# Kernel tuning notes

Measured on AMD Instinct MI355X. Metric: run time of the kernel, lower is better.

## Reference

```python
import jax, jax.numpy as jnp
import numpy as np

HIDDEN = 2048
N_HEADS = 16
N_KV = 2
HEAD_DIM = HIDDEN // N_HEADS  # 128


def setup_inputs() -> dict:
    key = jax.random.key(0)
    ks = jax.random.split(key, 9)
    s = 0.02
    kv_dim = N_KV * HEAD_DIM
    return {
        "hidden_states": jax.random.normal(ks[0], (2, 2048, HIDDEN), jnp.float32),
        "Wq": jax.random.normal(ks[1], (HIDDEN, HIDDEN), jnp.float32) * s,
        "bq": jnp.zeros((HIDDEN,), jnp.float32),
        "Wk": jax.random.normal(ks[2], (HIDDEN, kv_dim), jnp.float32) * s,
        "bk": jnp.zeros((kv_dim,), jnp.float32),
        "Wv": jax.random.normal(ks[3], (HIDDEN, kv_dim), jnp.float32) * s,
        "bv": jnp.zeros((kv_dim,), jnp.float32),
        "Wo": jax.random.normal(ks[4], (HIDDEN, HIDDEN), jnp.float32) * s,
        "bo": jnp.zeros((HIDDEN,), jnp.float32),
    }


def reference(hidden_states, Wq, bq, Wk, bk, Wv, bv, Wo, bo):
    B, S, _ = hidden_states.shape
    scaling = HEAD_DIM ** (-0.5)
    rep = N_HEADS // N_KV

    q = hidden_states @ Wq + bq                      # [B,S,H*D]
    k = hidden_states @ Wk + bk                      # [B,S,KV*D]
    v = hidden_states @ Wv + bv

    q = q.reshape(B, S, N_HEADS, HEAD_DIM) * scaling
    k = k.reshape(B, S, N_KV, HEAD_DIM)
    v = v.reshape(B, S, N_KV, HEAD_DIM)
    # repeat_interleave KV heads to match query heads (faithful to source)
    k = jnp.repeat(k, rep, axis=2)                   # [B,S,H,D]
    v = jnp.repeat(v, rep, axis=2)

    attn = jnp.einsum('bqhd,bkhd->bhqk', q, k)       # [B,H,S,S] score matrix
    attn = jax.nn.softmax(attn, axis=-1)
    out = jnp.einsum('bhqk,bkhd->bqhd', attn, v)     # [B,S,H,D]
    out = out.reshape(B, S, N_HEADS * HEAD_DIM)
    return out @ Wo + bo
```

## Files before the change

### kernel.cpp

```cpp
#include <hip/hip_runtime.h>

typedef __bf16 bf16;
typedef __bf16 bf16x4 __attribute__((ext_vector_type(4)));
typedef __bf16 bf16x8 __attribute__((ext_vector_type(8)));
typedef float  f32x4  __attribute__((ext_vector_type(4)));

#define AS1 __attribute__((address_space(1)))
#define AS3 __attribute__((address_space(3)))

__device__ __forceinline__ void gload_lds16(const void* g, void* l) {
    __builtin_amdgcn_global_load_lds((const AS1 void*)g, (AS3 void*)l, 16, 0, 0);
}

__global__ __launch_bounds__(256) void prep(
    const float* __restrict__ X,  const float* __restrict__ Wq,
    const float* __restrict__ Wk, const float* __restrict__ Wv,
    const float* __restrict__ Wo, const float* __restrict__ bq,
    const float* __restrict__ bk, const float* __restrict__ bv,
    bf16* __restrict__ Xb, bf16* __restrict__ Wqkvt,
    bf16* __restrict__ Wot, float* __restrict__ bqkv)
{
    __shared__ float tile[32][33];
    int bid = blockIdx.x;
    if (bid < 8192) {
        int i = bid * 256 + threadIdx.x;
        float4 v = ((const float4*)X)[i];
        bf16x4 o = { (bf16)v.x, (bf16)v.y, (bf16)v.z, (bf16)v.w };
        ((bf16x4*)Xb)[i] = o;
        return;
    }
    bid -= 8192;
    const float* src; bf16* dst; int R, C, bx, by;
    if (bid < 4096)      { src = Wq; dst = Wqkvt;                      R = 2048; C = 2048; bx = bid & 63; by = bid >> 6; }
    else if (bid < 4608) { int t = bid - 4096; src = Wk; dst = Wqkvt + (size_t)2048 * 2048; R = 2048; C = 256; bx = t & 7; by = t >> 3; }
    else if (bid < 5120) { int t = bid - 4608; src = Wv; dst = Wqkvt + (size_t)2304 * 2048; R = 2048; C = 256; bx = t & 7; by = t >> 3; }
    else if (bid < 9216) { int t = bid - 5120; src = Wo; dst = Wot;    R = 2048; C = 2048; bx = t & 63; by = t >> 6; }
    else {
        int i = (bid - 9216) * 256 + threadIdx.x;
        if (i < 2048) bqkv[i] = bq[i];
        else if (i < 2304) bqkv[i] = bk[i - 2048];
        else if (i < 2560) bqkv[i] = bv[i - 2304];
        return;
    }
    int tx = threadIdx.x & 31, tg = threadIdx.x >> 5;
    int c0 = bx * 32, r0 = by * 32;
    #pragma unroll
    for (int j = tg; j < 32; j += 8)
        tile[j][tx] = src[(size_t)(r0 + j) * C + c0 + tx];
    __syncthreads();
    #pragma unroll
    for (int j = tg; j < 32; j += 8)
        dst[(size_t)(c0 + j) * R + r0 + tx] = (bf16)tile[tx][j];
}

template<int OUTBF>
__global__ __launch_bounds__(256) void gemm_bt(
    const bf16* __restrict__ A, const bf16* __restrict__ Bt,
    const float* __restrict__ bias, void* __restrict__ Cv,
    int M, int N, int K, float scale)
{
    __shared__ bf16 As[128 * 32];
    __shared__ bf16 Bs[128 * 32];
    const int tid = threadIdx.x;
    const int l = tid & 63, w = tid >> 6;
    const int wm = w >> 1, wn = w & 1;
    const size_t rowBase = (size_t)blockIdx.y * 128;
    const size_t colBase = (size_t)blockIdx.x * 128;

    f32x4 acc[4][4] = {};

    const int srow = l >> 2;
    const int schunk = (l & 3) ^ ((l >> 3) & 3);
    const int frow = l & 15;
    const int fswz = (frow >> 1) & 3;
    const int g = l >> 4;

    const bf16* Ag = A  + (rowBase + w * 32 + srow) * (size_t)K + schunk * 8;
    const bf16* Bg = Bt + (colBase + w * 32 + srow) * (size_t)K + schunk * 8;

    for (int k0 = 0; k0 < K; k0 += 32) {
        gload_lds16(Ag + k0,                  As + (w * 32) * 32);
        gload_lds16(Ag + 16 * (size_t)K + k0, As + (w * 32 + 16) * 32);
        gload_lds16(Bg + k0,                  Bs + (w * 32) * 32);
        gload_lds16(Bg + 16 * (size_t)K + k0, Bs + (w * 32 + 16) * 32);
        __syncthreads();

        bf16x8 af[4], bfr[4];
        #pragma unroll
        for (int mi = 0; mi < 4; ++mi)
            af[mi] = *(const bf16x8*)(As + (wm * 64 + mi * 16 + frow) * 32 + ((g ^ fswz) << 3));
        #pragma unroll
        for (int ni = 0; ni < 4; ++ni)
            bfr[ni] = *(const bf16x8*)(Bs + (wn * 64 + ni * 16 + frow) * 32 + ((g ^ fswz) << 3));
        #pragma unroll
        for (int mi = 0; mi < 4; ++mi)
            #pragma unroll
            for (int ni = 0; ni < 4; ++ni)
                acc[mi][ni] = __builtin_amdgcn_mfma_f32_16x16x32_bf16(af[mi], bfr[ni], acc[mi][ni], 0, 0, 0);
        __syncthreads();
    }

    const int cr = (l >> 4) * 4;
    const int cc = l & 15;
    #pragma unroll
    for (int ni = 0; ni < 4; ++ni) {
        const int col = (int)colBase + wn * 64 + ni * 16 + cc;
        const float bv = bias[col];
        #pragma unroll
        for (int mi = 0; mi < 4; ++mi) {
            #pragma unroll
            for (int r = 0; r < 4; ++r) {
                const size_t row = rowBase + wm * 64 + mi * 16 + cr + r;
                float v = (acc[mi][ni][r] + bv) * scale;
                if (OUTBF) ((bf16*)Cv)[row * N + col] = (bf16)v;
                else       ((float*)Cv)[row * N + col] = v;
            }
        }
    }
}

__global__ __launch_bounds__(256) void gemm_qkv(
    const bf16* __restrict__ A, const bf16* __restrict__ Bt,
    const float* __restrict__ bias, bf16* __restrict__ Qb, bf16* __restrict__ Kb,
    bf16* __restrict__ VT, float qscale)
{
    constexpr int K = 2048;
    __shared__ bf16 As[128 * 32];
    __shared__ bf16 Bs[128 * 32];
    const int tid = threadIdx.x;
    const int l = tid & 63, w = tid >> 6;
    const int wm = w >> 1, wn = w & 1;
    const size_t rowBase = (size_t)blockIdx.y * 128;
    const size_t colBase = (size_t)blockIdx.x * 128;

    f32x4 acc[4][4] = {};

    const int srow = l >> 2;
    const int schunk = (l & 3) ^ ((l >> 3) & 3);
    const int frow = l & 15;
    const int fswz = (frow >> 1) & 3;
    const int g = l >> 4;

    const bf16* Ag = A  + (rowBase + w * 32 + srow) * (size_t)K + schunk * 8;
    const bf16* Bg = Bt + (colBase + w * 32 + srow) * (size_t)K + schunk * 8;

    for (int k0 = 0; k0 < K; k0 += 32) {
        gload_lds16(Ag + k0,                  As + (w * 32) * 32);
        gload_lds16(Ag + 16 * (size_t)K + k0, As + (w * 32 + 16) * 32);
        gload_lds16(Bg + k0,                  Bs + (w * 32) * 32);
        gload_lds16(Bg + 16 * (size_t)K + k0, Bs + (w * 32 + 16) * 32);
        __syncthreads();

        bf16x8 af[4], bfr[4];
        #pragma unroll
        for (int mi = 0; mi < 4; ++mi)
            af[mi] = *(const bf16x8*)(As + (wm * 64 + mi * 16 + frow) * 32 + ((g ^ fswz) << 3));
        #pragma unroll
        for (int ni = 0; ni < 4; ++ni)
            bfr[ni] = *(const bf16x8*)(Bs + (wn * 64 + ni * 16 + frow) * 32 + ((g ^ fswz) << 3));
        #pragma unroll
        for (int mi = 0; mi < 4; ++mi)
            #pragma unroll
            for (int ni = 0; ni < 4; ++ni)
                acc[mi][ni] = __builtin_amdgcn_mfma_f32_16x16x32_bf16(af[mi], bfr[ni], acc[mi][ni], 0, 0, 0);
        __syncthreads();
    }

    const int cr = (l >> 4) * 4;
    const int cc = l & 15;
    const int cb = (int)colBase;
    #pragma unroll
    for (int ni = 0; ni < 4; ++ni) {
        const int col = cb + wn * 64 + ni * 16 + cc;
        const float bv = bias[col];
        if (cb < 2048) {
            #pragma unroll
            for (int mi = 0; mi < 4; ++mi)
                #pragma unroll
                for (int r = 0; r < 4; ++r) {
                    const size_t row = rowBase + wm * 64 + mi * 16 + cr + r;
                    Qb[row * 2048 + col] = (bf16)((acc[mi][ni][r] + bv) * qscale);
                }
        } else if (cb < 2304) {
            #pragma unroll
            for (int mi = 0; mi < 4; ++mi)
                #pragma unroll
                for (int r = 0; r < 4; ++r) {
                    const size_t row = rowBase + wm * 64 + mi * 16 + cr + r;
                    Kb[row * 256 + (col - 2048)] = (bf16)(acc[mi][ni][r] + bv);
                }
        } else {
            const int vcol = col - 2304;
            const int kvh = vcol >> 7, d = vcol & 127;
            #pragma unroll
            for (int mi = 0; mi < 4; ++mi) {
                const size_t row0 = rowBase + wm * 64 + mi * 16 + cr;
                const int bb = (int)(row0 >> 11);
                const int s  = (int)(row0 & 2047);
                const int tile = s >> 6, sp = s & 63;
                const int slot = (sp & 35) | ((sp & 8) << 1) | ((sp & 4) << 1) | ((sp & 16) >> 2);
                bf16x4 v4 = { (bf16)(acc[mi][ni][0] + bv), (bf16)(acc[mi][ni][1] + bv),
                              (bf16)(acc[mi][ni][2] + bv), (bf16)(acc[mi][ni][3] + bv) };
                *(bf16x4*)(VT + ((size_t)((bb * 2 + kvh) * 128 + d)) * 2048 + tile * 64 + slot) = v4;
            }
        }
    }
}

__global__ __launch_bounds__(512, 4) void attn_fwd(
    const bf16* __restrict__ Q, const bf16* __restrict__ Kb,
    const bf16* __restrict__ VT, bf16* __restrict__ O)
{
    constexpr int S = 2048;
    constexpr int NT = S / 64;
    extern __shared__ bf16 smem[];
    bf16* Ks = smem;
    bf16* Vs = smem + 16384;

    const int tid = threadIdx.x;
    const int l = tid & 63, w = tid >> 6;
    const int qt = blockIdx.x, h = blockIdx.y, b = blockIdx.z;
    const int kvh = h >> 3;
    const int lg = l >> 4, ll = l & 15;
    const int eh = (ll >> 2) & 1;

    bf16x8 qf[4];
    {
        const bf16* qp = Q + ((size_t)(b * S + qt * 128 + w * 16 + ll)) * 2048 + h * 128 + lg * 8;
        #pragma unroll
        for (int j = 0; j < 4; ++j) qf[j] = *(const bf16x8*)(qp + (j << 5));
    }

    const bf16* Kg  = Kb + (size_t)b * S * 256 + kvh * 128;
    const bf16* VTg = VT + ((size_t)(b * 2 + kvh) * 128) * S;

    const bf16* kg0 = Kg + (size_t)(w * 8 + lg) * 256 + (ll ^ lg) * 8;
    const bf16* kg1 = Kg + (size_t)(w * 8 + 4 + lg) * 256 + (ll ^ (4 + lg)) * 8;
    const bf16* vg0 = VTg + (size_t)(w * 16 + (l >> 3)) * S + (((l & 7) ^ ((l >> 3) & 7)) << 3);
    const bf16* vg1 = vg0 + 8 * (size_t)S;
    const int kd0 = (w * 8) * 128;
    const int kd1 = (w * 8 + 4) * 128;
    const int vd0 = w * 1024;
    const int vd1 = w * 1024 + 512;

    const int swz8 = (lg ^ (ll & 3)) << 3;
    const int kbE = ll * 128 + swz8 + eh * 32;
    const int kbO = ll * 128 + swz8 + (1 - eh) * 32;
    const int vbE = ll * 64 + swz8 + eh * 32;
    const int vbO = ll * 64 + swz8 + (1 - eh) * 32;

    bf16x8 vones;
    #pragma unroll
    for (int e = 0; e < 8; ++e) vones[e] = (bf16)1.0f;

    f32x4 of[8] = {};
    f32x4 of_l = {};
    bf16x8 paA, paB;

    gload_lds16(kg0, Ks + kd0);
    gload_lds16(kg1, Ks + kd1);
    gload_lds16(vg0, Vs + vd0);
    gload_lds16(vg1, Vs + vd1);
    __syncthreads();

    int sP = 2, sC = 0, sN = 1;
    for (int t = 0; t < NT; ++t) {
        const int buf = t & 1;
        if (t + 1 < NT) {
            const size_t ko = (size_t)(t + 1) * 64 * 256;
            const int    vo = (t + 1) * 64;
            gload_lds16(kg0 + ko, Ks + (buf ^ 1) * 8192 + kd0);
            gload_lds16(kg1 + ko, Ks + (buf ^ 1) * 8192 + kd1);
            gload_lds16(vg0 + vo, Vs + sN * 8192 + vd0);
            gload_lds16(vg1 + vo, Vs + sN * 8192 + vd1);
        }

        const bf16* kE = Ks + buf * 8192 + kbE;
        const bf16* kO = Ks + buf * 8192 + kbO;
        f32x4 sc[4] = {};
        __builtin_amdgcn_s_setprio(1);
        #pragma unroll
        for (int ni = 0; ni < 4; ++ni) {
            bf16x8 k0f = *(const bf16x8*)(kE + ni * 2048);
            sc[ni] = __builtin_amdgcn_mfma_f32_16x16x32_bf16(k0f, qf[0], sc[ni], 0, 0, 0);
            bf16x8 k1f = *(const bf16x8*)(kO + ni * 2048);
            sc[ni] = __builtin_amdgcn_mfma_f32_16x16x32_bf16(k1f, qf[1], sc[ni], 0, 0, 0);
            bf16x8 k2f = *(const bf16x8*)(kE + ni * 2048 + 64);
            sc[ni] = __builtin_amdgcn_mfma_f32_16x16x32_bf16(k2f, qf[2], sc[ni], 0, 0, 0);
            bf16x8 k3f = *(const bf16x8*)(kO + ni * 2048 + 64);
            sc[ni] = __builtin_amdgcn_mfma_f32_16x16x32_bf16(k3f, qf[3], sc[ni], 0, 0, 0);
        }
        __builtin_amdgcn_s_setprio(0);

        if (t > 0) {
            const bf16* vE = Vs + sP * 8192 + vbE;
            const bf16* vO = Vs + sP * 8192 + vbO;
            __builtin_amdgcn_s_setprio(1);
            of_l = __builtin_amdgcn_mfma_f32_16x16x32_bf16(paA, vones, of_l, 0, 0, 0);
            #pragma unroll
            for (int nf = 0; nf < 8; ++nf) {
                bf16x8 v0 = *(const bf16x8*)(vE + nf * 1024);
                of[nf] = __builtin_amdgcn_mfma_f32_16x16x32_bf16(paA, v0, of[nf], 0, 0, 0);
            }
            of_l = __builtin_amdgcn_mfma_f32_16x16x32_bf16(paB, vones, of_l, 0, 0, 0);
            #pragma unroll
            for (int nf = 0; nf < 8; ++nf) {
                bf16x8 v1 = *(const bf16x8*)(vO + nf * 1024);
                of[nf] = __builtin_amdgcn_mfma_f32_16x16x32_bf16(paB, v1, of[nf], 0, 0, 0);
            }
            __builtin_amdgcn_s_setprio(0);
        }

        float p[4][4];
        #pragma unroll
        for (int ni = 0; ni < 4; ++ni)
            #pragma unroll
            for (int r = 0; r < 4; ++r)
                p[ni][r] = __builtin_exp2f(sc[ni][r]);
        bf16x8 npa0, npa1;
        #pragma unroll
        for (int e = 0; e < 8; ++e) {
            npa0[e] = (bf16)p[(e >> 2)][e & 3];
            npa1[e] = (bf16)p[2 + (e >> 2)][e & 3];
        }
        paA = npa0; paB = npa1;

        __syncthreads();
        int tmp = sP; sP = sC; sC = sN; sN = tmp;
    }

    {
        const bf16* vE = Vs + sP * 8192 + vbE;
        const bf16* vO = Vs + sP * 8192 + vbO;
        of_l = __builtin_amdgcn_mfma_f32_16x16x32_bf16(paA, vones, of_l, 0, 0, 0);
        #pragma unroll
        for (int nf = 0; nf < 8; ++nf) {
            bf16x8 v0 = *(const bf16x8*)(vE + nf * 1024);
            of[nf] = __builtin_amdgcn_mfma_f32_16x16x32_bf16(paA, v0, of[nf], 0, 0, 0);
        }
        of_l = __builtin_amdgcn_mfma_f32_16x16x32_bf16(paB, vones, of_l, 0, 0, 0);
        #pragma unroll
        for (int nf = 0; nf < 8; ++nf) {
            bf16x8 v1 = *(const bf16x8*)(vO + nf * 1024);
            of[nf] = __builtin_amdgcn_mfma_f32_16x16x32_bf16(paB, v1, of[nf], 0, 0, 0);
        }
    }

    #pragma unroll
    for (int r = 0; r < 4; ++r) {
        float inv = 1.0f / of_l[r];
        size_t row = (size_t)(b * S + qt * 128 + w * 16 + lg * 4 + r);
        bf16* op = O + row * 2048 + h * 128 + ll;
        #pragma unroll
        for (int nf = 0; nf < 8; ++nf)
            op[nf * 16] = (bf16)(of[nf][r] * inv);
    }
}

extern "C" void kernel_launch(void* const* d_in, const int* in_sizes, int n_in,
                              void* d_out, int out_size, void* d_ws, size_t ws_size,
                              hipStream_t stream)
{
    const float* X  = (const float*)d_in[0];
    const float* Wq = (const float*)d_in[1];
    const float* bq = (const float*)d_in[2];
    const float* Wk = (const float*)d_in[3];
    const float* bk = (const float*)d_in[4];
    const float* Wv = (const float*)d_in[5];
    const float* bv = (const float*)d_in[6];
    const float* Wo = (const float*)d_in[7];
    const float* bo = (const float*)d_in[8];
    float* out = (float*)d_out;

    bf16* p = (bf16*)d_ws;
    bf16* Xb    = p; p += 8388608;
    bf16* Qb    = p; p += 8388608;
    bf16* Kbuf  = p; p += 1048576;
    bf16* VTb   = p; p += 1048576;
    bf16* Wqkvt = p; p += 5242880;
    bf16* Wot   = p; p += 4194304;
    float* bqkv = (float*)p; p += 5120;
    bf16* Oattn = Xb;

    const float qscale = 0.12751744f;

    (void)hipFuncSetAttribute((const void*)attn_fwd,
                              hipFuncAttributeMaxDynamicSharedMemorySize, 81920);

    prep<<<17418, 256, 0, stream>>>(X, Wq, Wk, Wv, Wo, bq, bk, bv,
                                    Xb, Wqkvt, Wot, bqkv);

    gemm_qkv<<<dim3(20, 32), 256, 0, stream>>>(Xb, Wqkvt, bqkv, Qb, Kbuf, VTb, qscale);

    attn_fwd<<<dim3(16, 16, 2), 512, 81920, stream>>>(Qb, Kbuf, VTb, Oattn);

    gemm_bt<0><<<dim3(16, 32), 256, 0, stream>>>(Oattn, Wot, bo, out, 4096, 2048, 2048, 1.0f);
}
```

Measured before the change: 202.9 us.

## Process two 16-row query tiles per wave to double K/V reuse in attention

Each attention wave now handles 32 query rows (two 16-row fragments) instead of 16, so every K and V fragment read from LDS feeds twice as many MFMAs. The grid is halved along the query dimension and the launch bound drops from 4 to 2 blocks per CU to leave room for the doubled accumulators and score registers. This cuts LDS read traffic and global K/V loads per query row. In exchange it lowers occupancy and launches only 256 blocks, which may underfill the GPU.

```diff
diff --git a/kernel.cpp b/kernel.cpp
--- a/kernel.cpp
+++ b/kernel.cpp
@@ -207,7 +207,7 @@
     }
 }
 
-__global__ __launch_bounds__(512, 4) void attn_fwd(
+__global__ __launch_bounds__(512, 2) void attn_fwd(
     const bf16* __restrict__ Q, const bf16* __restrict__ Kb,
     const bf16* __restrict__ VT, bf16* __restrict__ O)
 {
@@ -224,11 +224,15 @@
     const int lg = l >> 4, ll = l & 15;
     const int eh = (ll >> 2) & 1;
 
-    bf16x8 qf[4];
+    bf16x8 qfA[4], qfB[4];
     {
-        const bf16* qp = Q + ((size_t)(b * S + qt * 128 + w * 16 + ll)) * 2048 + h * 128 + lg * 8;
-        #pragma unroll
-        for (int j = 0; j < 4; ++j) qf[j] = *(const bf16x8*)(qp + (j << 5));
+        const bf16* qpA = Q + ((size_t)(b * S + qt * 256 + w * 32 + ll)) * 2048 + h * 128 + lg * 8;
+        const bf16* qpB = qpA + 16 * 2048;
+        #pragma unroll
+        for (int j = 0; j < 4; ++j) {
+            qfA[j] = *(const bf16x8*)(qpA + (j << 5));
+            qfB[j] = *(const bf16x8*)(qpB + (j << 5));
+        }
     }
 
     const bf16* Kg  = Kb + (size_t)b * S * 256 + kvh * 128;
@@ -253,9 +257,9 @@
     #pragma unroll
     for (int e = 0; e < 8; ++e) vones[e] = (bf16)1.0f;
 
-    f32x4 of[8] = {};
-    f32x4 of_l = {};
-    bf16x8 paA, paB;
+    f32x4 ofA[8] = {}, ofB[8] = {};
+    f32x4 olA = {}, olB = {};
+    bf16x8 pA0, pA1, pB0, pB1;
 
     gload_lds16(kg0, Ks + kd0);
     gload_lds16(kg1, Ks + kd1);
@@ -277,18 +281,22 @@
 
         const bf16* kE = Ks + buf * 8192 + kbE;
         const bf16* kO = Ks + buf * 8192 + kbO;
-        f32x4 sc[4] = {};
+        f32x4 scA[4] = {}, scB[4] = {};
         __builtin_amdgcn_s_setprio(1);
         #pragma unroll
         for (int ni = 0; ni < 4; ++ni) {
             bf16x8 k0f = *(const bf16x8*)(kE + ni * 2048);
-            sc[ni] = __builtin_amdgcn_mfma_f32_16x16x32_bf16(k0f, qf[0], sc[ni], 0, 0, 0);
+            scA[ni] = __builtin_amdgcn_mfma_f32_16x16x32_bf16(k0f, qfA[0], scA[ni], 0, 0, 0);
+            scB[ni] = __builtin_amdgcn_mfma_f32_16x16x32_bf16(k0f, qfB[0], scB[ni], 0, 0, 0);
             bf16x8 k1f = *(const bf16x8*)(kO + ni * 2048);
-            sc[ni] = __builtin_amdgcn_mfma_f32_16x16x32_bf16(k1f, qf[1], sc[ni], 0, 0, 0);
+            scA[ni] = __builtin_amdgcn_mfma_f32_16x16x32_bf16(k1f, qfA[1], scA[ni], 0, 0, 0);
+            scB[ni] = __builtin_amdgcn_mfma_f32_16x16x32_bf16(k1f, qfB[1], scB[ni], 0, 0, 0);
             bf16x8 k2f = *(const bf16x8*)(kE + ni * 2048 + 64);
-            sc[ni] = __builtin_amdgcn_mfma_f32_16x16x32_bf16(k2f, qf[2], sc[ni], 0, 0, 0);
+            scA[ni] = __builtin_amdgcn_mfma_f32_16x16x32_bf16(k2f, qfA[2], scA[ni], 0, 0, 0);
+            scB[ni] = __builtin_amdgcn_mfma_f32_16x16x32_bf16(k2f, qfB[2], scB[ni], 0, 0, 0);
             bf16x8 k3f = *(const bf16x8*)(kO + ni * 2048 + 64);
-            sc[ni] = __builtin_amdgcn_mfma_f32_16x16x32_bf16(k3f, qf[3], sc[ni], 0, 0, 0);
+            scA[ni] = __builtin_amdgcn_mfma_f32_16x16x32_bf16(k3f, qfA[3], scA[ni], 0, 0, 0);
+            scB[ni] = __builtin_amdgcn_mfma_f32_16x16x32_bf16(k3f, qfB[3], scB[ni], 0, 0, 0);
         }
         __builtin_amdgcn_s_setprio(0);
 
@@ -296,34 +304,40 @@
             const bf16* vE = Vs + sP * 8192 + vbE;
             const bf16* vO = Vs + sP * 8192 + vbO;
             __builtin_amdgcn_s_setprio(1);
-            of_l = __builtin_amdgcn_mfma_f32_16x16x32_bf16(paA, vones, of_l, 0, 0, 0);
+            olA = __builtin_amdgcn_mfma_f32_16x16x32_bf16(pA0, vones, olA, 0, 0, 0);
+            olB = __builtin_amdgcn_mfma_f32_16x16x32_bf16(pB0, vones, olB, 0, 0, 0);
             #pragma unroll
             for (int nf = 0; nf < 8; ++nf) {
                 bf16x8 v0 = *(const bf16x8*)(vE + nf * 1024);
-                of[nf] = __builtin_amdgcn_mfma_f32_16x16x32_bf16(paA, v0, of[nf], 0, 0, 0);
+                ofA[nf] = __builtin_amdgcn_mfma_f32_16x16x32_bf16(pA0, v0, ofA[nf], 0, 0, 0);
+                ofB[nf] = __builtin_amdgcn_mfma_f32_16x16x32_bf16(pB0, v0, ofB[nf], 0, 0, 0);
             }
-            of_l = __builtin_amdgcn_mfma_f32_16x16x32_bf16(paB, vones, of_l, 0, 0, 0);
+            olA = __builtin_amdgcn_mfma_f32_16x16x32_bf16(pA1, vones, olA, 0, 0, 0);
+            olB = __builtin_amdgcn_mfma_f32_16x16x32_bf16(pB1, vones, olB, 0, 0, 0);
             #pragma unroll
             for (int nf = 0; nf < 8; ++nf) {
                 bf16x8 v1 = *(const bf16x8*)(vO + nf * 1024);
-                of[nf] = __builtin_amdgcn_mfma_f32_16x16x32_bf16(paB, v1, of[nf], 0, 0, 0);
+                ofA[nf] = __builtin_amdgcn_mfma_f32_16x16x32_bf16(pA1, v1, ofA[nf], 0, 0, 0);
+                ofB[nf] = __builtin_amdgcn_mfma_f32_16x16x32_bf16(pB1, v1, ofB[nf], 0, 0, 0);
             }
             __builtin_amdgcn_s_setprio(0);
         }
 
-        float p[4][4];
+        float pa[4][4], pb[4][4];
         #pragma unroll
         for (int ni = 0; ni < 4; ++ni)
             #pragma unroll
-            for (int r = 0; r < 4; ++r)
-                p[ni][r] = __builtin_exp2f(sc[ni][r]);
-        bf16x8 npa0, npa1;
+            for (int r = 0; r < 4; ++r) {
+                pa[ni][r] = __builtin_exp2f(scA[ni][r]);
+                pb[ni][r] = __builtin_exp2f(scB[ni][r]);
+            }
         #pragma unroll
         for (int e = 0; e < 8; ++e) {
-            npa0[e] = (bf16)p[(e >> 2)][e & 3];
-            npa1[e] = (bf16)p[2 + (e >> 2)][e & 3];
-        }
-        paA = npa0; paB = npa1;
+            pA0[e] = (bf16)pa[(e >> 2)][e & 3];
+            pA1[e] = (bf16)pa[2 + (e >> 2)][e & 3];
+            pB0[e] = (bf16)pb[(e >> 2)][e & 3];
+            pB1[e] = (bf16)pb[2 + (e >> 2)][e & 3];
+        }
 
         __syncthreads();
         int tmp = sP; sP = sC; sC = sN; sN = tmp;
@@ -332,28 +346,36 @@
     {
         const bf16* vE = Vs + sP * 8192 + vbE;
         const bf16* vO = Vs + sP * 8192 + vbO;
-        of_l = __builtin_amdgcn_mfma_f32_16x16x32_bf16(paA, vones, of_l, 0, 0, 0);
+        olA = __builtin_amdgcn_mfma_f32_16x16x32_bf16(pA0, vones, olA, 0, 0, 0);
+        olB = __builtin_amdgcn_mfma_f32_16x16x32_bf16(pB0, vones, olB, 0, 0, 0);
         #pragma unroll
         for (int nf = 0; nf < 8; ++nf) {
             bf16x8 v0 = *(const bf16x8*)(vE + nf * 1024);
-            of[nf] = __builtin_amdgcn_mfma_f32_16x16x32_bf16(paA, v0, of[nf], 0, 0, 0);
-        }
-        of_l = __builtin_amdgcn_mfma_f32_16x16x32_bf16(paB, vones, of_l, 0, 0, 0);
+            ofA[nf] = __builtin_amdgcn_mfma_f32_16x16x32_bf16(pA0, v0, ofA[nf], 0, 0, 0);
+            ofB[nf] = __builtin_amdgcn_mfma_f32_16x16x32_bf16(pB0, v0, ofB[nf], 0, 0, 0);
+        }
+        olA = __builtin_amdgcn_mfma_f32_16x16x32_bf16(pA1, vones, olA, 0, 0, 0);
+        olB = __builtin_amdgcn_mfma_f32_16x16x32_bf16(pB1, vones, olB, 0, 0, 0);
         #pragma unroll
         for (int nf = 0; nf < 8; ++nf) {
             bf16x8 v1 = *(const bf16x8*)(vO + nf * 1024);
-            of[nf] = __builtin_amdgcn_mfma_f32_16x16x32_bf16(paB, v1, of[nf], 0, 0, 0);
+            ofA[nf] = __builtin_amdgcn_mfma_f32_16x16x32_bf16(pA1, v1, ofA[nf], 0, 0, 0);
+            ofB[nf] = __builtin_amdgcn_mfma_f32_16x16x32_bf16(pB1, v1, ofB[nf], 0, 0, 0);
         }
     }
 
     #pragma unroll
     for (int r = 0; r < 4; ++r) {
-        float inv = 1.0f / of_l[r];
-        size_t row = (size_t)(b * S + qt * 128 + w * 16 + lg * 4 + r);
-        bf16* op = O + row * 2048 + h * 128 + ll;
-        #pragma unroll
-        for (int nf = 0; nf < 8; ++nf)
-            op[nf * 16] = (bf16)(of[nf][r] * inv);
+        float invA = 1.0f / olA[r];
+        float invB = 1.0f / olB[r];
+        size_t rowA = (size_t)(b * S + qt * 256 + w * 32 + lg * 4 + r);
+        bf16* opA = O + rowA * 2048 + h * 128 + ll;
+        bf16* opB = opA + 16 * 2048;
+        #pragma unroll
+        for (int nf = 0; nf < 8; ++nf) {
+            opA[nf * 16] = (bf16)(ofA[nf][r] * invA);
+            opB[nf * 16] = (bf16)(ofB[nf][r] * invB);
+        }
     }
 }
 
@@ -392,7 +414,7 @@
 
     gemm_qkv<<<dim3(20, 32), 256, 0, stream>>>(Xb, Wqkvt, bqkv, Qb, Kbuf, VTb, qscale);
 
-    attn_fwd<<<dim3(16, 16, 2), 512, 81920, stream>>>(Qb, Kbuf, VTb, Oattn);
+    attn_fwd<<<dim3(8, 16, 2), 512, 81920, stream>>>(Qb, Kbuf, VTb, Oattn);
 
     gemm_bt<0><<<dim3(16, 32), 256, 0, stream>>>(Oattn, Wot, bo, out, 4096, 2048, 2048, 1.0f);
 }
```

Measured after the change: 200.5 us. Within noise of the previous version (-1.2%).
